# Optimization experiments

Measured on AMD Instinct MI355X. Metric: run time of the kernel, lower is better.

## Reference

```python
import jax, jax.numpy as jnp
import numpy as np

LN_EPS = 1e-5

def setup_inputs() -> dict:
    key = jax.random.key(0)
    ks = jax.random.split(key, 16)
    B, N = 16384, 1000000
    return {
        "user_input": jax.random.randint(ks[0], (B,), 0, N),
        "emb": jax.random.normal(ks[1], (N, 64), jnp.float32),
        "sc_country_idx": jax.random.randint(ks[2], (N,), 0, 256),
        "sc_country_emb": jax.random.normal(ks[3], (256, 32), jnp.float32),
        "sc_device_idx": jax.random.randint(ks[4], (N,), 0, 10000),
        "sc_device_emb": jax.random.normal(ks[5], (10000, 32), jnp.float32),
        "mf_tags_idx": jax.random.randint(ks[6], (N, 20), 0, 50000),
        "mf_tags_emb": jax.random.normal(ks[7], (50000, 32), jnp.float32),
        "mf_history_idx": jax.random.randint(ks[8], (N, 50), 0, 100000),
        "mf_history_emb": jax.random.normal(ks[9], (100000, 32), jnp.float32),
        "fc_w": jax.random.normal(ks[10], (256, 192), jnp.float32) * 0.05,
        "fc_b": jax.random.normal(ks[11], (256,), jnp.float32) * 0.05,
        "ln_g": jnp.ones((256,), jnp.float32),
        "ln_b": jnp.zeros((256,), jnp.float32),
    }

def _layernorm(x, g, b):
    mu = jnp.mean(x, axis=-1, keepdims=True)
    var = jnp.mean(jnp.square(x - mu), axis=-1, keepdims=True)
    return (x - mu) * jax.lax.rsqrt(var + LN_EPS) * g + b

def reference(user_input, emb, sc_country_idx, sc_country_emb, sc_device_idx, sc_device_emb,
               mf_tags_idx, mf_tags_emb, mf_history_idx, mf_history_emb,
               fc_w, fc_b, ln_g, ln_b):
    parts = [emb[user_input]]  # [B, 64]
    # scalar side features: buffer lookup then embedding gather -> [B, 32]
    parts.append(sc_country_emb[sc_country_idx[user_input]])
    parts.append(sc_device_emb[sc_device_idx[user_input]])
    # multi-valued side features: [B, W] index lists -> gather -> mean pool -> [B, 32]
    parts.append(jnp.mean(mf_tags_emb[mf_tags_idx[user_input]], axis=1))
    parts.append(jnp.mean(mf_history_emb[mf_history_idx[user_input]], axis=1))
    x = jnp.concatenate(parts, axis=-1)  # [B, 192]
    x = jax.nn.relu(x @ fc_w.T + fc_b)   # [B, 256]
    return _layernorm(x, ln_g, ln_b)
```

## Files before the change

kernel.cpp:

```cpp
#include <hip/hip_runtime.h>

#define LN_EPS 1e-5f

constexpr int KDIM = 192;
constexpr int NOUT = 256;
constexpr int ROWS_PER_BLOCK = 32;
constexpr int ROWS_PER_WAVE  = 8;

__global__ __launch_bounds__(256)
void ut_gather_kernel(const int*   __restrict__ user_input,
                      const float* __restrict__ emb,
                      const int*   __restrict__ sc_country_idx,
                      const float* __restrict__ sc_country_emb,
                      const int*   __restrict__ sc_device_idx,
                      const float* __restrict__ sc_device_emb,
                      const int*   __restrict__ mf_tags_idx,
                      const float* __restrict__ mf_tags_emb,
                      const int*   __restrict__ mf_history_idx,
                      const float* __restrict__ mf_history_emb,
                      float*       __restrict__ X,
                      int B)
{
    const int lane = threadIdx.x & 63;
    const int wave = threadIdx.x >> 6;
    const int row  = blockIdx.x * 4 + wave;
    if (row >= B) return;

    const int half = lane >> 5;
    const int col  = lane & 31;
    const int jt   = lane >> 3;
    const int fc   = lane & 7;

    const int u = __builtin_amdgcn_readfirstlane(user_input[row]);
    float* __restrict__ Xr = X + (size_t)row * KDIM;

    const int ci = sc_country_idx[u];
    const int di = sc_device_idx[u];

    const int* __restrict__ tp = mf_tags_idx    + (size_t)u * 20;
    const int* __restrict__ hp = mf_history_idx + (size_t)u * 50;

    int  ti[3];  bool tv[3];
    #pragma unroll
    for (int p = 0; p < 3; ++p) {
        const int j = p * 8 + jt;
        tv[p] = (j < 20);
        ti[p] = tv[p] ? tp[j] : 0;
    }
    int  hi[7];  bool hv[7];
    #pragma unroll
    for (int p = 0; p < 7; ++p) {
        const int j = p * 8 + jt;
        hv[p] = (j < 50);
        hi[p] = hv[p] ? hp[j] : 0;
    }

    const float e = emb[(size_t)u * 64 + lane];

    const float sc = (half == 0) ? sc_country_emb[ci * 32 + col]
                                 : sc_device_emb [di * 32 + col];

    float4 ta4 = make_float4(0.f, 0.f, 0.f, 0.f);
    #pragma unroll
    for (int p = 0; p < 3; ++p) {
        const float4 g = *(const float4*)&mf_tags_emb[(size_t)ti[p] * 32 + fc * 4];
        if (tv[p]) { ta4.x += g.x; ta4.y += g.y; ta4.z += g.z; ta4.w += g.w; }
    }
    float4 ha4 = make_float4(0.f, 0.f, 0.f, 0.f);
    #pragma unroll
    for (int p = 0; p < 7; ++p) {
        const float4 g = *(const float4*)&mf_history_emb[(size_t)hi[p] * 32 + fc * 4];
        if (hv[p]) { ha4.x += g.x; ha4.y += g.y; ha4.z += g.z; ha4.w += g.w; }
    }

    #pragma unroll
    for (int m = 8; m <= 32; m <<= 1) {
        ta4.x += __shfl_xor(ta4.x, m, 64);  ta4.y += __shfl_xor(ta4.y, m, 64);
        ta4.z += __shfl_xor(ta4.z, m, 64);  ta4.w += __shfl_xor(ta4.w, m, 64);
        ha4.x += __shfl_xor(ha4.x, m, 64);  ha4.y += __shfl_xor(ha4.y, m, 64);
        ha4.z += __shfl_xor(ha4.z, m, 64);  ha4.w += __shfl_xor(ha4.w, m, 64);
    }

    Xr[lane] = e;
    if (half == 0) Xr[64 + col] = sc;
    else           Xr[96 + col] = sc;
    if (lane < 8) {
        const float s_t = 1.f / 20.f, s_h = 1.f / 50.f;
        float4 t = make_float4(ta4.x * s_t, ta4.y * s_t, ta4.z * s_t, ta4.w * s_t);
        float4 h = make_float4(ha4.x * s_h, ha4.y * s_h, ha4.z * s_h, ha4.w * s_h);
        *(float4*)&Xr[128 + lane * 4] = t;
        *(float4*)&Xr[160 + lane * 4] = h;
    }
}

__global__ __launch_bounds__(256)
void ut_fc_ln_kernel(const float* __restrict__ Xg,
                     const float* __restrict__ fc_w,
                     const float* __restrict__ fc_b,
                     const float* __restrict__ ln_g,
                     const float* __restrict__ ln_b,
                     float*       __restrict__ out,
                     int B)
{
    __shared__ float X[ROWS_PER_BLOCK][KDIM];

    const int tid  = threadIdx.x;
    const int lane = tid & 63;
    const int wave = tid >> 6;
    const int row0 = blockIdx.x * ROWS_PER_BLOCK;

    {
        const float4* __restrict__ src = (const float4*)(Xg + (size_t)row0 * KDIM);
        float4* dst = (float4*)&X[0][0];
        #pragma unroll
        for (int i = 0; i < 6; ++i) dst[tid + 256 * i] = src[tid + 256 * i];
    }
    __syncthreads();

    const int c0 = lane;
    float acc[ROWS_PER_WAVE][4];
    float g4[4], b4[4];
    #pragma unroll
    for (int ci = 0; ci < 4; ++ci) {
        const int c = c0 + 64 * ci;
        const float bias = fc_b[c];
        g4[ci] = ln_g[c];
        b4[ci] = ln_b[c];
        #pragma unroll
        for (int ri = 0; ri < ROWS_PER_WAVE; ++ri) acc[ri][ci] = bias;
    }

    for (int kc = 0; kc < KDIM; kc += 4) {
        float4 w[4];
        #pragma unroll
        for (int ci = 0; ci < 4; ++ci)
            w[ci] = *(const float4*)&fc_w[(c0 + 64 * ci) * KDIM + kc];
        #pragma unroll
        for (int ri = 0; ri < ROWS_PER_WAVE; ++ri) {
            const float4 x = *(const float4*)&X[wave * ROWS_PER_WAVE + ri][kc];
            #pragma unroll
            for (int ci = 0; ci < 4; ++ci) {
                acc[ri][ci] += x.x * w[ci].x + x.y * w[ci].y
                             + x.z * w[ci].z + x.w * w[ci].w;
            }
        }
    }

    #pragma unroll
    for (int ri = 0; ri < ROWS_PER_WAVE; ++ri) {
        const int row = row0 + wave * ROWS_PER_WAVE + ri;
        float y[4];
        float s = 0.f, s2 = 0.f;
        #pragma unroll
        for (int ci = 0; ci < 4; ++ci) {
            y[ci] = fmaxf(acc[ri][ci], 0.f);
            s  += y[ci];
            s2 += y[ci] * y[ci];
        }
        #pragma unroll
        for (int m = 32; m >= 1; m >>= 1) {
            s  += __shfl_xor(s,  m, 64);
            s2 += __shfl_xor(s2, m, 64);
        }
        const float mu  = s  * (1.f / 256.f);
        const float var = s2 * (1.f / 256.f) - mu * mu;
        const float rs  = rsqrtf(var + LN_EPS);
        if (row < B) {
            #pragma unroll
            for (int ci = 0; ci < 4; ++ci) {
                const int c = c0 + 64 * ci;
                out[row * NOUT + c] = (y[ci] - mu) * rs * g4[ci] + b4[ci];
            }
        }
    }
}

extern "C" void kernel_launch(void* const* d_in, const int* in_sizes, int n_in,
                              void* d_out, int out_size, void* d_ws, size_t ws_size,
                              hipStream_t stream)
{
    const int*   user_input     = (const int*)  d_in[0];
    const float* emb            = (const float*)d_in[1];
    const int*   sc_country_idx = (const int*)  d_in[2];
    const float* sc_country_emb = (const float*)d_in[3];
    const int*   sc_device_idx  = (const int*)  d_in[4];
    const float* sc_device_emb  = (const float*)d_in[5];
    const int*   mf_tags_idx    = (const int*)  d_in[6];
    const float* mf_tags_emb    = (const float*)d_in[7];
    const int*   mf_history_idx = (const int*)  d_in[8];
    const float* mf_history_emb = (const float*)d_in[9];
    const float* fc_w           = (const float*)d_in[10];
    const float* fc_b           = (const float*)d_in[11];
    const float* ln_g           = (const float*)d_in[12];
    const float* ln_b           = (const float*)d_in[13];
    float*       out            = (float*)d_out;
    float*       X              = (float*)d_ws;

    const int B = in_sizes[0];

    const int gatherGrid = (B + 3) / 4;
    ut_gather_kernel<<<gatherGrid, 256, 0, stream>>>(
        user_input, emb, sc_country_idx, sc_country_emb,
        sc_device_idx, sc_device_emb, mf_tags_idx, mf_tags_emb,
        mf_history_idx, mf_history_emb, X, B);

    const int fcGrid = (B + ROWS_PER_BLOCK - 1) / ROWS_PER_BLOCK;
    ut_fc_ln_kernel<<<fcGrid, 256, 0, stream>>>(
        X, fc_w, fc_b, ln_g, ln_b, out, B);
}
```

Baseline: 519.0 us.

## Use fp16 MFMA for FC layer with half-precision intermediate and weights

```diff
diff --git a/kernel.cpp b/kernel.cpp
--- a/kernel.cpp
+++ b/kernel.cpp
@@ -1,11 +1,23 @@
 #include <hip/hip_runtime.h>
 
 #define LN_EPS 1e-5f
+
+typedef _Float16 f16;
+typedef _Float16 f16x4 __attribute__((ext_vector_type(4)));
+typedef _Float16 f16x8 __attribute__((ext_vector_type(8)));
+typedef float    f32x4 __attribute__((ext_vector_type(4)));
 
 constexpr int KDIM = 192;
 constexpr int NOUT = 256;
-constexpr int ROWS_PER_BLOCK = 32;
-constexpr int ROWS_PER_WAVE  = 8;
+
+__global__ __launch_bounds__(256)
+void ut_wconv_kernel(const float* __restrict__ fc_w, f16* __restrict__ W16)
+{
+    const int i = blockIdx.x * 256 + threadIdx.x;
+    const float4 v = ((const float4*)fc_w)[i];
+    f16x4 h = { (f16)v.x, (f16)v.y, (f16)v.z, (f16)v.w };
+    ((f16x4*)W16)[i] = h;
+}
 
 __global__ __launch_bounds__(256)
 void ut_gather_kernel(const int*   __restrict__ user_input,
@@ -18,7 +30,7 @@
                       const float* __restrict__ mf_tags_emb,
                       const int*   __restrict__ mf_history_idx,
                       const float* __restrict__ mf_history_emb,
-                      float*       __restrict__ X,
+                      f16*         __restrict__ X16,
                       int B)
 {
     const int lane = threadIdx.x & 63;
@@ -32,7 +44,7 @@
     const int fc   = lane & 7;
 
     const int u = __builtin_amdgcn_readfirstlane(user_input[row]);
-    float* __restrict__ Xr = X + (size_t)row * KDIM;
+    f16* __restrict__ Xr = X16 + (size_t)row * KDIM;
 
     const int ci = sc_country_idx[u];
     const int di = sc_device_idx[u];
@@ -81,96 +93,109 @@
         ha4.z += __shfl_xor(ha4.z, m, 64);  ha4.w += __shfl_xor(ha4.w, m, 64);
     }
 
-    Xr[lane] = e;
-    if (half == 0) Xr[64 + col] = sc;
-    else           Xr[96 + col] = sc;
+    Xr[lane] = (f16)e;
+    if (half == 0) Xr[64 + col] = (f16)sc;
+    else           Xr[96 + col] = (f16)sc;
     if (lane < 8) {
         const float s_t = 1.f / 20.f, s_h = 1.f / 50.f;
-        float4 t = make_float4(ta4.x * s_t, ta4.y * s_t, ta4.z * s_t, ta4.w * s_t);
-        float4 h = make_float4(ha4.x * s_h, ha4.y * s_h, ha4.z * s_h, ha4.w * s_h);
-        *(float4*)&Xr[128 + lane * 4] = t;
-        *(float4*)&Xr[160 + lane * 4] = h;
+        f16x4 t = { (f16)(ta4.x * s_t), (f16)(ta4.y * s_t),
+                    (f16)(ta4.z * s_t), (f16)(ta4.w * s_t) };
+        f16x4 h = { (f16)(ha4.x * s_h), (f16)(ha4.y * s_h),
+                    (f16)(ha4.z * s_h), (f16)(ha4.w * s_h) };
+        *(f16x4*)&Xr[128 + lane * 4] = t;
+        *(f16x4*)&Xr[160 + lane * 4] = h;
     }
 }
 
 __global__ __launch_bounds__(256)
-void ut_fc_ln_kernel(const float* __restrict__ Xg,
-                     const float* __restrict__ fc_w,
+void ut_fc_ln_kernel(const f16*   __restrict__ X16,
+                     const f16*   __restrict__ W16,
                      const float* __restrict__ fc_b,
                      const float* __restrict__ ln_g,
                      const float* __restrict__ ln_b,
                      float*       __restrict__ out,
                      int B)
 {
-    __shared__ float X[ROWS_PER_BLOCK][KDIM];
+    __shared__ float sb[4][16];
+    __shared__ float s2b[4][16];
 
     const int tid  = threadIdx.x;
     const int lane = tid & 63;
     const int wave = tid >> 6;
-    const int row0 = blockIdx.x * ROWS_PER_BLOCK;
-
-    {
-        const float4* __restrict__ src = (const float4*)(Xg + (size_t)row0 * KDIM);
-        float4* dst = (float4*)&X[0][0];
-        #pragma unroll
-        for (int i = 0; i < 6; ++i) dst[tid + 256 * i] = src[tid + 256 * i];
+    const int t    = lane & 15;
+    const int quad = lane >> 4;
+    const int row0 = blockIdx.x * 16;
+    if (row0 >= B) return;
+    const int colbase = wave * 64;
+
+    const f16* __restrict__ arow = X16 + (size_t)(row0 + t) * KDIM + quad * 8;
+
+    f32x4 acc[4];
+    #pragma unroll
+    for (int ct = 0; ct < 4; ++ct) acc[ct] = (f32x4){0.f, 0.f, 0.f, 0.f};
+
+    #pragma unroll
+    for (int kt = 0; kt < 6; ++kt) {
+        const f16x8 a = *(const f16x8*)(arow + kt * 32);
+        #pragma unroll
+        for (int ct = 0; ct < 4; ++ct) {
+            const f16x8 b = *(const f16x8*)(W16 + (size_t)(colbase + ct * 16 + t) * KDIM
+                                                 + kt * 32 + quad * 8);
+            acc[ct] = __builtin_amdgcn_mfma_f32_16x16x32_f16(a, b, acc[ct], 0, 0, 0);
+        }
+    }
+
+    float bias[4], g4[4], bb4[4];
+    #pragma unroll
+    for (int ct = 0; ct < 4; ++ct) {
+        const int c = colbase + ct * 16 + t;
+        bias[ct] = fc_b[c];
+        g4[ct]   = ln_g[c];
+        bb4[ct]  = ln_b[c];
+    }
+
+    float y[4][4];
+    float s[4]  = {0.f, 0.f, 0.f, 0.f};
+    float s2[4] = {0.f, 0.f, 0.f, 0.f};
+    #pragma unroll
+    for (int ct = 0; ct < 4; ++ct) {
+        #pragma unroll
+        for (int r = 0; r < 4; ++r) {
+            const float v = fmaxf(acc[ct][r] + bias[ct], 0.f);
+            y[ct][r] = v;
+            s[r]  += v;
+            s2[r] += v * v;
+        }
+    }
+    #pragma unroll
+    for (int m = 1; m <= 8; m <<= 1) {
+        #pragma unroll
+        for (int r = 0; r < 4; ++r) {
+            s[r]  += __shfl_xor(s[r],  m, 64);
+            s2[r] += __shfl_xor(s2[r], m, 64);
+        }
+    }
+    if (t == 0) {
+        #pragma unroll
+        for (int r = 0; r < 4; ++r) {
+            sb [wave][quad * 4 + r] = s[r];
+            s2b[wave][quad * 4 + r] = s2[r];
+        }
     }
     __syncthreads();
 
-    const int c0 = lane;
-    float acc[ROWS_PER_WAVE][4];
-    float g4[4], b4[4];
-    #pragma unroll
-    for (int ci = 0; ci < 4; ++ci) {
-        const int c = c0 + 64 * ci;
-        const float bias = fc_b[c];
-        g4[ci] = ln_g[c];
-        b4[ci] = ln_b[c];
-        #pragma unroll
-        for (int ri = 0; ri < ROWS_PER_WAVE; ++ri) acc[ri][ci] = bias;
-    }
-
-    for (int kc = 0; kc < KDIM; kc += 4) {
-        float4 w[4];
-        #pragma unroll
-        for (int ci = 0; ci < 4; ++ci)
-            w[ci] = *(const float4*)&fc_w[(c0 + 64 * ci) * KDIM + kc];
-        #pragma unroll
-        for (int ri = 0; ri < ROWS_PER_WAVE; ++ri) {
-            const float4 x = *(const float4*)&X[wave * ROWS_PER_WAVE + ri][kc];
-            #pragma unroll
-            for (int ci = 0; ci < 4; ++ci) {
-                acc[ri][ci] += x.x * w[ci].x + x.y * w[ci].y
-                             + x.z * w[ci].z + x.w * w[ci].w;
-            }
-        }
-    }
-
-    #pragma unroll
-    for (int ri = 0; ri < ROWS_PER_WAVE; ++ri) {
-        const int row = row0 + wave * ROWS_PER_WAVE + ri;
-        float y[4];
-        float s = 0.f, s2 = 0.f;
-        #pragma unroll
-        for (int ci = 0; ci < 4; ++ci) {
-            y[ci] = fmaxf(acc[ri][ci], 0.f);
-            s  += y[ci];
-            s2 += y[ci] * y[ci];
-        }
-        #pragma unroll
-        for (int m = 32; m >= 1; m >>= 1) {
-            s  += __shfl_xor(s,  m, 64);
-            s2 += __shfl_xor(s2, m, 64);
-        }
-        const float mu  = s  * (1.f / 256.f);
-        const float var = s2 * (1.f / 256.f) - mu * mu;
+    #pragma unroll
+    for (int r = 0; r < 4; ++r) {
+        const int rho = quad * 4 + r;
+        const float st  = sb [0][rho] + sb [1][rho] + sb [2][rho] + sb [3][rho];
+        const float s2t = s2b[0][rho] + s2b[1][rho] + s2b[2][rho] + s2b[3][rho];
+        const float mu  = st  * (1.f / 256.f);
+        const float var = s2t * (1.f / 256.f) - mu * mu;
         const float rs  = rsqrtf(var + LN_EPS);
-        if (row < B) {
-            #pragma unroll
-            for (int ci = 0; ci < 4; ++ci) {
-                const int c = c0 + 64 * ci;
-                out[row * NOUT + c] = (y[ci] - mu) * rs * g4[ci] + b4[ci];
-            }
+        #pragma unroll
+        for (int ct = 0; ct < 4; ++ct) {
+            const int c = colbase + ct * 16 + t;
+            out[(size_t)(row0 + rho) * NOUT + c] = (y[ct][r] - mu) * rs * g4[ct] + bb4[ct];
         }
     }
 }
@@ -194,17 +219,21 @@
     const float* ln_g           = (const float*)d_in[12];
     const float* ln_b           = (const float*)d_in[13];
     float*       out            = (float*)d_out;
-    float*       X              = (float*)d_ws;
+
+    f16* X16 = (f16*)d_ws;
+    f16* W16 = (f16*)((char*)d_ws + (size_t)(16 << 20));
 
     const int B = in_sizes[0];
+
+    ut_wconv_kernel<<<48, 256, 0, stream>>>(fc_w, W16);
 
     const int gatherGrid = (B + 3) / 4;
     ut_gather_kernel<<<gatherGrid, 256, 0, stream>>>(
         user_input, emb, sc_country_idx, sc_country_emb,
         sc_device_idx, sc_device_emb, mf_tags_idx, mf_tags_emb,
-        mf_history_idx, mf_history_emb, X, B);
-
-    const int fcGrid = (B + ROWS_PER_BLOCK - 1) / ROWS_PER_BLOCK;
+        mf_history_idx, mf_history_emb, X16, B);
+
+    const int fcGrid = (B + 15) / 16;
     ut_fc_ln_kernel<<<fcGrid, 256, 0, stream>>>(
-        X, fc_w, fc_b, ln_g, ln_b, out, B);
-}
+        X16, W16, fc_b, ln_g, ln_b, out, B);
+}
```

New measurement: 466.0 us. 1.11x faster.
